# Performance work log

Hardware: AMD Instinct MI355X
Metric: run time of the kernel (lower is better)

Reference implementation:

```python
import jax, jax.numpy as jnp
import numpy as np

UNITS = 2048
BATCH = 4096
INPUT_DIM = 2048

def hard_sigmoid(x):
    # Keras hard_sigmoid: clip(0.2*x + 0.5, 0, 1)
    return jnp.clip(0.2 * x + 0.5, 0.0, 1.0)

def setup_inputs() -> dict:
    key = jax.random.key(0)
    ks = jax.random.split(key, 8)
    inputs = jax.random.normal(ks[0], (BATCH, INPUT_DIM), dtype=jnp.float32)
    h_tm1 = jax.random.normal(ks[1], (BATCH, UNITS), dtype=jnp.float32)
    c_tm1 = jax.random.normal(ks[2], (BATCH, UNITS), dtype=jnp.float32)
    z_tm1 = jax.random.normal(ks[3], (BATCH, UNITS), dtype=jnp.float32)
    scale = 1.0 / np.sqrt(INPUT_DIM)
    kernel = jax.random.normal(ks[4], (INPUT_DIM, 4 * UNITS), dtype=jnp.float32) * scale
    recurrent_kernel = jax.random.normal(ks[5], (UNITS, 4 * UNITS), dtype=jnp.float32) * scale
    recurrent_latent = jax.random.normal(ks[6], (UNITS, 4 * UNITS), dtype=jnp.float32) * scale
    # unit_forget_bias: bias = [zeros(units), ones(units), zeros(2*units)]
    bias = jnp.concatenate([
        jnp.zeros((UNITS,), jnp.float32),
        jnp.ones((UNITS,), jnp.float32),
        jnp.zeros((2 * UNITS,), jnp.float32),
    ])
    return {"inputs": inputs, "h_tm1": h_tm1, "c_tm1": c_tm1, "z_tm1": z_tm1,
            "kernel": kernel, "recurrent_kernel": recurrent_kernel,
            "recurrent_latent": recurrent_latent, "bias": bias}

def reference(inputs, h_tm1, c_tm1, z_tm1, kernel, recurrent_kernel, recurrent_latent, bias):
    # Fused path (implementation=2, no dropout): three matmuls + bias,
    # split into 4 gates, then gated state update.
    x = inputs @ kernel + h_tm1 @ recurrent_kernel + z_tm1 @ recurrent_latent + bias
    x_i, x_f, x_c, x_o = jnp.split(x, 4, axis=1)
    i = hard_sigmoid(x_i)
    f = hard_sigmoid(x_f)
    c = f * c_tm1 + i * jnp.tanh(x_c)
    o = hard_sigmoid(x_o)
    h = o * jnp.tanh(c)
    return h
```

## Files before the change

### kernel.cpp

```cpp
#include <hip/hip_runtime.h>
#include <hip/hip_bf16.h>

typedef float f32x4 __attribute__((ext_vector_type(4)));
typedef short short8 __attribute__((ext_vector_type(8)));
typedef short short4v __attribute__((ext_vector_type(4)));

__device__ __forceinline__ short f2b(float x) {
    union { __hip_bfloat16 b; short s; } u;
    u.b = __float2bfloat16(x);
    return u.s;
}

__device__ __forceinline__ void gload16(const void* g, void* l) {
    __builtin_amdgcn_global_load_lds(
        (const __attribute__((address_space(1))) unsigned int*)g,
        (__attribute__((address_space(3))) unsigned int*)l, 16, 0, 0);
}

__global__ __launch_bounds__(256)
void conv_a(const float* __restrict__ x0, const float* __restrict__ x1,
            const float* __restrict__ x2, unsigned short* __restrict__ Aws)
{
    const long i = (long)blockIdx.x * 256 + threadIdx.x;
    const long per_src = (long)4096 * 2048 / 8;
    const int  s = (int)(i / per_src);
    const long e0 = (i % per_src) * 8;
    const int  row = (int)(e0 >> 11), kl = (int)(e0 & 2047);
    const float* src = (s == 0) ? x0 : (s == 1) ? x1 : x2;
    const f32x4 v0 = *(const f32x4*)(src + e0);
    const f32x4 v1 = *(const f32x4*)(src + e0 + 4);
    short8 p;
    #pragma unroll
    for (int j = 0; j < 4; ++j) { p[j] = f2b(v0[j]); p[4 + j] = f2b(v1[j]); }
    *(short8*)&Aws[(long)row * 6144 + s * 2048 + kl] = p;
}

__global__ __launch_bounds__(256)
void conv_b(const float* __restrict__ Wk, const float* __restrict__ Wr,
            const float* __restrict__ Wl, unsigned short* __restrict__ Bws)
{
    __shared__ float lt[64][65];
    const int bid = (int)blockIdx.x;
    const int s   = bid >> 12;
    const int r   = bid & 4095;
    const int kbase = (r >> 7) * 64;
    const int ebase = (r & 127) * 64;
    const float* W = (s == 0) ? Wk : (s == 1) ? Wr : Wl;
    const int tr = threadIdx.x >> 4, tc = threadIdx.x & 15;

    #pragma unroll
    for (int p = 0; p < 4; ++p) {
        const int kr = p * 16 + tr;
        const f32x4 v = *(const f32x4*)&W[(long)(kbase + kr) * 8192 + ebase + tc * 4];
        #pragma unroll
        for (int j = 0; j < 4; ++j) lt[kr][tc * 4 + j] = v[j];
    }
    __syncthreads();
    #pragma unroll
    for (int p = 0; p < 4; ++p) {
        const int er = p * 16 + tr;
        const int k4 = tc * 4;
        short4v qv;
        #pragma unroll
        for (int j = 0; j < 4; ++j) qv[j] = f2b(lt[k4 + j][er]);
        *(short4v*)&Bws[(long)(ebase + er) * 6144 + (long)s * 2048 + kbase + k4] = qv;
    }
}

__global__ __launch_bounds__(512, 2)
void vlstm_gemm256(const unsigned short* __restrict__ Aws,
                   const unsigned short* __restrict__ Bws,
                   const float* __restrict__ c_tm1,
                   const float* __restrict__ bias,
                   float* __restrict__ out)
{
    __shared__ __align__(16) unsigned short As[2][256][64];
    __shared__ __align__(16) unsigned short Bs[3][256][64];

    const int tid  = threadIdx.x;
    const int w    = tid >> 6, lane = tid & 63;
    const int wm   = w >> 2,  wn   = w & 3;
    const int l15  = lane & 15, q = lane >> 4;
    const int lrow = lane >> 3;
    const int lsw  = (lane & 7) ^ lrow;
    const int oq   = q ^ (l15 & 7);

    const int bid = (int)blockIdx.x;
    const int swz = (bid & 7) * 64 + (bid >> 3);
    const int bm  = swz >> 5, bn = swz & 31;
    const int row0 = bm * 256, c0 = bn * 64;

    const long a_base = (long)(row0 + w * 16 + lrow) * 6144 + lsw * 8;

    f32x4 acc[8][4];
    #pragma unroll
    for (int mi = 0; mi < 8; ++mi)
        #pragma unroll
        for (int g = 0; g < 4; ++g)
            acc[mi][g] = (f32x4){0.f, 0.f, 0.f, 0.f};

    short8 afr[4][2];
    short8 bfr[4][2];

#define STAGE_A(buf_, t_, h_) do { _Pragma("unroll")                             \
    for (int j_ = 0; j_ < 2; ++j_)                                               \
        gload16(Aws + a_base + (long)((h_) * 128 + j_ * 8) * 6144                \
                    + (long)(t_) * 64,                                           \
                &As[buf_][(h_) * 128 + w * 16 + j_ * 8][0]); } while (0)

#define STAGE_B(buf_, t_, h_) do { _Pragma("unroll")                             \
    for (int j_ = 0; j_ < 2; ++j_) {                                             \
        const int e0_ = (h_) * 128 + w * 16 + j_ * 8;                            \
        const int grow_ = ((e0_ >> 4) & 3) * 2048 + c0 + (e0_ >> 6) * 16         \
                          + (e0_ & 8) + lrow;                                    \
        gload16(Bws + (long)grow_ * 6144 + lsw * 8 + (long)(t_) * 64,            \
                &Bs[buf_][e0_][0]); } } while (0)

#define LOAD_AFR(cur_, mh_) do { _Pragma("unroll")                               \
    for (int mi_ = 0; mi_ < 4; ++mi_) { _Pragma("unroll")                        \
        for (int kh_ = 0; kh_ < 2; ++kh_)                                        \
            afr[mi_][kh_] = *(const short8*)                                     \
                &As[cur_][wm * 128 + (mh_) * 64 + mi_ * 16 + l15]                \
                         [(oq ^ (kh_ << 2)) * 8]; } } while (0)

#define LOAD_BFR(cur_, nlo_) do { _Pragma("unroll")                              \
    for (int g_ = 0; g_ < 2; ++g_) { _Pragma("unroll")                           \
        for (int kh_ = 0; kh_ < 2; ++kh_)                                        \
            bfr[(nlo_) + g_][kh_] = *(const short8*)                             \
                &Bs[cur_][wn * 64 + ((nlo_) + g_) * 16 + l15]                    \
                         [(oq ^ (kh_ << 2)) * 8]; } } while (0)

#define MFMA_Q(mh_, nlo_) do {                                                   \
    __builtin_amdgcn_s_setprio(1);                                               \
    _Pragma("unroll")                                                            \
    for (int kh_ = 0; kh_ < 2; ++kh_) { _Pragma("unroll")                        \
        for (int mi_ = 0; mi_ < 4; ++mi_) { _Pragma("unroll")                    \
            for (int g_ = 0; g_ < 2; ++g_)                                       \
                acc[(mh_) * 4 + mi_][(nlo_) + g_] =                              \
                    __builtin_amdgcn_mfma_f32_16x16x32_bf16(                     \
                        afr[mi_][kh_], bfr[(nlo_) + g_][kh_],                    \
                        acc[(mh_) * 4 + mi_][(nlo_) + g_], 0, 0, 0); } }         \
    __builtin_amdgcn_s_setprio(0); } while (0)

#define BARRIER() do { __builtin_amdgcn_sched_barrier(0);                        \
    __builtin_amdgcn_s_barrier();                                                \
    __builtin_amdgcn_sched_barrier(0); } while (0)

    STAGE_A(0, 0, 0); STAGE_A(0, 0, 1);
    STAGE_B(0, 0, 0); STAGE_B(0, 0, 1);
    STAGE_B(1, 1, 0); STAGE_B(1, 1, 1);
    asm volatile("s_waitcnt vmcnt(4)" ::: "memory");
    BARRIER();

    int bB = 0;
    for (int t = 0; t < 96; ++t) {
        const int bA = t & 1, bAn = bA ^ 1;
        const int bBs = bB ? bB - 1 : 2;
        LOAD_AFR(bA, 0);
        LOAD_BFR(bB, 0);
        if (t + 1 < 96) STAGE_A(bAn, t + 1, 0);
        MFMA_Q(0, 0);
        LOAD_BFR(bB, 2);
        if (t + 1 < 96) STAGE_A(bAn, t + 1, 1);
        MFMA_Q(0, 2);
        LOAD_AFR(bA, 1);
        if (t + 2 < 96) STAGE_B(bBs, t + 2, 0);
        MFMA_Q(1, 0);
        if (t + 2 < 96) STAGE_B(bBs, t + 2, 1);
        MFMA_Q(1, 2);
        if (t < 94) asm volatile("s_waitcnt vmcnt(4)" ::: "memory");
        else        asm volatile("s_waitcnt vmcnt(0)" ::: "memory");
        BARRIER();
        bB = (bB == 2) ? 0 : bB + 1;
    }

#undef STAGE_A
#undef STAGE_B
#undef LOAD_AFR
#undef LOAD_BFR
#undef MFMA_Q
#undef BARRIER

    {
        const int col = c0 + wn * 16 + l15;
        const float bi  = bias[col];
        const float bf_ = bias[2048 + col];
        const float bc  = bias[4096 + col];
        const float bo  = bias[6144 + col];
        #pragma unroll
        for (int mi = 0; mi < 8; ++mi) {
            const int rbase = row0 + wm * 128 + mi * 16 + q * 4;
            #pragma unroll
            for (int rr = 0; rr < 4; ++rr) {
                const int row = rbase + rr;
                const float xi = acc[mi][0][rr] + bi;
                const float xf = acc[mi][1][rr] + bf_;
                const float xc = acc[mi][2][rr] + bc;
                const float xo = acc[mi][3][rr] + bo;
                const float ig = __builtin_amdgcn_fmed3f(0.2f * xi + 0.5f, 0.f, 1.f);
                const float fg = __builtin_amdgcn_fmed3f(0.2f * xf + 0.5f, 0.f, 1.f);
                const float og = __builtin_amdgcn_fmed3f(0.2f * xo + 0.5f, 0.f, 1.f);
                const float cp = c_tm1[(long)row * 2048 + col];
                const float cc = fg * cp + ig * tanhf(xc);
                out[(long)row * 2048 + col] = og * tanhf(cc);
            }
        }
    }
}

__global__ __launch_bounds__(256, 2)
void vlstm_fused_legacy(const float* __restrict__ xin, const float* __restrict__ h_tm1,
                        const float* __restrict__ c_tm1, const float* __restrict__ z_tm1,
                        const float* __restrict__ Wk, const float* __restrict__ Wr,
                        const float* __restrict__ Wl, const float* __restrict__ bias,
                        float* __restrict__ out)
{
    __shared__ __align__(16) unsigned short Alds[2][128][40];
    __shared__ __align__(16) unsigned short Blds[2][256][40];

    const int tid  = threadIdx.x;
    const int wave = tid >> 6, lane = tid & 63;
    const int wr = wave >> 1, wc = wave & 1;
    const int l15 = lane & 15, q = lane >> 4;

    const int bid = (int)blockIdx.x;
    const int swz = (bid & 7) * 128 + (bid >> 3);
    const int bm = swz >> 5, bn = swz & 31;
    const int row0 = bm * 128, col0 = bn * 64;

    const int arow = tid >> 1, kh = tid & 1;
    const long bg_off = (long)(tid >> 6) * 2048 + col0 + (tid & 63);

    f32x4 acc[4][4][2];
    #pragma unroll
    for (int g = 0; g < 4; ++g)
        #pragma unroll
        for (int mi = 0; mi < 4; ++mi)
            #pragma unroll
            for (int ni = 0; ni < 2; ++ni)
                acc[g][mi][ni] = (f32x4){0.f, 0.f, 0.f, 0.f};

    f32x4 sa[4];
    float sb[32];

#define DO_LOADS_L(kn_) do {                                                    \
    const int s_  = (kn_) >> 6;                                                 \
    const int kl_ = ((kn_) & 63) << 5;                                          \
    const float* Ap_ = (s_ == 0) ? xin : (s_ == 1) ? h_tm1 : z_tm1;             \
    const float* Bp_ = (s_ == 0) ? Wk  : (s_ == 1) ? Wr    : Wl;                \
    const float* ap_ = Ap_ + (long)(row0 + arow) * 2048 + kl_ + kh * 16;        \
    _Pragma("unroll")                                                           \
    for (int i_ = 0; i_ < 4; ++i_) sa[i_] = ((const f32x4*)ap_)[i_];            \
    const float* bp_ = Bp_ + (long)kl_ * 8192 + bg_off;                         \
    _Pragma("unroll")                                                           \
    for (int kk_ = 0; kk_ < 32; ++kk_) sb[kk_] = bp_[(long)kk_ * 8192];         \
} while (0)

#define DO_STORE_L(buf_) do {                                                   \
    short8 p0_, p1_;                                                            \
    _Pragma("unroll")                                                           \
    for (int j_ = 0; j_ < 4; ++j_) {                                            \
        p0_[j_] = f2b(sa[0][j_]); p0_[4 + j_] = f2b(sa[1][j_]);                 \
        p1_[j_] = f2b(sa[2][j_]); p1_[4 + j_] = f2b(sa[3][j_]);                 \
    }                                                                           \
    *(short8*)&Alds[buf_][arow][kh * 16]     = p0_;                             \
    *(short8*)&Alds[buf_][arow][kh * 16 + 8] = p1_;                             \
    _Pragma("unroll")                                                           \
    for (int ks_ = 0; ks_ < 4; ++ks_) {                                         \
        short8 pb_;                                                             \
        _Pragma("unroll")                                                       \
        for (int j_ = 0; j_ < 8; ++j_) pb_[j_] = f2b(sb[ks_ * 8 + j_]);         \
        *(short8*)&Blds[buf_][tid][ks_ * 8] = pb_;                              \
    }                                                                           \
} while (0)

    DO_LOADS_L(0);
    DO_STORE_L(0);
    __syncthreads();

    for (int kt = 0; kt < 192; ++kt) {
        const int cur = kt & 1;
        if (kt + 1 < 192) DO_LOADS_L(kt + 1);

        short8 afr[4];
        #pragma unroll
        for (int mi = 0; mi < 4; ++mi)
            afr[mi] = *(const short8*)&Alds[cur][wr * 64 + mi * 16 + l15][q * 8];

        short8 bfr[4][2];
        #pragma unroll
        for (int g = 0; g < 4; ++g)
            #pragma unroll
            for (int ni = 0; ni < 2; ++ni)
                bfr[g][ni] = *(const short8*)
                    &Blds[cur][g * 64 + wc * 32 + ni * 16 + l15][q * 8];

        #pragma unroll
        for (int g = 0; g < 4; ++g)
            #pragma unroll
            for (int ni = 0; ni < 2; ++ni)
                #pragma unroll
                for (int mi = 0; mi < 4; ++mi)
                    acc[g][mi][ni] = __builtin_amdgcn_mfma_f32_16x16x32_bf16(
                        afr[mi], bfr[g][ni], acc[g][mi][ni], 0, 0, 0);

        if (kt + 1 < 192) DO_STORE_L(cur ^ 1);
        __syncthreads();
    }

#undef DO_LOADS_L
#undef DO_STORE_L

    #pragma unroll
    for (int ni = 0; ni < 2; ++ni) {
        const int col = col0 + wc * 32 + ni * 16 + l15;
        const float bi  = bias[col];
        const float bf_ = bias[2048 + col];
        const float bc  = bias[4096 + col];
        const float bo  = bias[6144 + col];
        #pragma unroll
        for (int mi = 0; mi < 4; ++mi) {
            const int rbase = row0 + wr * 64 + mi * 16 + q * 4;
            #pragma unroll
            for (int rr = 0; rr < 4; ++rr) {
                const int row = rbase + rr;
                const float xi = acc[0][mi][ni][rr] + bi;
                const float xf = acc[1][mi][ni][rr] + bf_;
                const float xc = acc[2][mi][ni][rr] + bc;
                const float xo = acc[3][mi][ni][rr] + bo;
                const float ig = __builtin_amdgcn_fmed3f(0.2f * xi + 0.5f, 0.f, 1.f);
                const float fg = __builtin_amdgcn_fmed3f(0.2f * xf + 0.5f, 0.f, 1.f);
                const float og = __builtin_amdgcn_fmed3f(0.2f * xo + 0.5f, 0.f, 1.f);
                const float cp = c_tm1[(long)row * 2048 + col];
                const float cc = fg * cp + ig * tanhf(xc);
                out[(long)row * 2048 + col] = og * tanhf(cc);
            }
        }
    }
}

extern "C" void kernel_launch(void* const* d_in, const int* in_sizes, int n_in,
                              void* d_out, int out_size, void* d_ws, size_t ws_size,
                              hipStream_t stream) {
    const float* xin  = (const float*)d_in[0];
    const float* h1   = (const float*)d_in[1];
    const float* c1   = (const float*)d_in[2];
    const float* z1   = (const float*)d_in[3];
    const float* Wk   = (const float*)d_in[4];
    const float* Wr   = (const float*)d_in[5];
    const float* Wl   = (const float*)d_in[6];
    const float* bias = (const float*)d_in[7];
    float* out = (float*)d_out;
    (void)in_sizes; (void)n_in; (void)out_size;

    const size_t a_elems = (size_t)4096 * 6144;
    const size_t b_elems = (size_t)8192 * 6144;
    const size_t need = (a_elems + b_elems) * 2;

    if (ws_size >= need) {
        unsigned short* Aws = (unsigned short*)d_ws;
        unsigned short* Bws = Aws + a_elems;
        conv_a<<<dim3(12288), dim3(256), 0, stream>>>(xin, h1, z1, Aws);
        conv_b<<<dim3(12288), dim3(256), 0, stream>>>(Wk, Wr, Wl, Bws);
        vlstm_gemm256<<<dim3(512), dim3(512), 0, stream>>>(Aws, Bws, c1, bias, out);
    } else {
        vlstm_fused_legacy<<<dim3(1024), dim3(256), 0, stream>>>(
            xin, h1, c1, z1, Wk, Wr, Wl, bias, out);
    }
}
```

Baseline: 497.9 us.

## Load B fragments directly from global into registers, dropping B LDS staging

B tiles are no longer staged through shared memory. Each wave now loads its B MFMA fragments straight from global memory into a double-buffered register bank (b0/b1), prefetched one K-step ahead, and the loop is unrolled by two to alternate the banks. This removes the 96KB Bs LDS buffer and the LDS reads for B, which could improve occupancy and cut LDS traffic. The cost is that the four waves sharing the same wn now each fetch the same B data redundantly from global/L2, and register pressure rises.

```diff
diff --git a/kernel.cpp b/kernel.cpp
--- a/kernel.cpp
+++ b/kernel.cpp
@@ -68,14 +68,13 @@
 }
 
 __global__ __launch_bounds__(512, 2)
-void vlstm_gemm256(const unsigned short* __restrict__ Aws,
+void vlstm_gemm_bd(const unsigned short* __restrict__ Aws,
                    const unsigned short* __restrict__ Bws,
                    const float* __restrict__ c_tm1,
                    const float* __restrict__ bias,
                    float* __restrict__ out)
 {
     __shared__ __align__(16) unsigned short As[2][256][64];
-    __shared__ __align__(16) unsigned short Bs[3][256][64];
 
     const int tid  = threadIdx.x;
     const int w    = tid >> 6, lane = tid & 63;
@@ -92,6 +91,14 @@
 
     const long a_base = (long)(row0 + w * 16 + lrow) * 6144 + lsw * 8;
 
+    const unsigned short* bpg[4];
+    {
+        const unsigned short* bp0 =
+            Bws + ((long)(c0 + wn * 16 + l15) * 6144 + q * 8);
+        #pragma unroll
+        for (int g = 0; g < 4; ++g) bpg[g] = bp0 + (long)g * (2048 * 6144);
+    }
+
     f32x4 acc[8][4];
     #pragma unroll
     for (int mi = 0; mi < 8; ++mi)
@@ -100,7 +107,7 @@
             acc[mi][g] = (f32x4){0.f, 0.f, 0.f, 0.f};
 
     short8 afr[4][2];
-    short8 bfr[4][2];
+    short8 b0[4][2], b1[4][2];
 
 #define STAGE_A(buf_, t_, h_) do { _Pragma("unroll")                             \
     for (int j_ = 0; j_ < 2; ++j_)                                               \
@@ -108,13 +115,11 @@
                     + (long)(t_) * 64,                                           \
                 &As[buf_][(h_) * 128 + w * 16 + j_ * 8][0]); } while (0)
 
-#define STAGE_B(buf_, t_, h_) do { _Pragma("unroll")                             \
-    for (int j_ = 0; j_ < 2; ++j_) {                                             \
-        const int e0_ = (h_) * 128 + w * 16 + j_ * 8;                            \
-        const int grow_ = ((e0_ >> 4) & 3) * 2048 + c0 + (e0_ >> 6) * 16         \
-                          + (e0_ & 8) + lrow;                                    \
-        gload16(Bws + (long)grow_ * 6144 + lsw * 8 + (long)(t_) * 64,            \
-                &Bs[buf_][e0_][0]); } } while (0)
+#define BLOADS(bank_, t_) do { _Pragma("unroll")                                 \
+    for (int g_ = 0; g_ < 4; ++g_) {                                             \
+        bank_[g_][0] = *(const short8*)(bpg[g_] + (long)(t_) * 64);              \
+        bank_[g_][1] = *(const short8*)(bpg[g_] + (long)(t_) * 64 + 32);         \
+    } } while (0)
 
 #define LOAD_AFR(cur_, mh_) do { _Pragma("unroll")                               \
     for (int mi_ = 0; mi_ < 4; ++mi_) { _Pragma("unroll")                        \
@@ -123,14 +128,7 @@
                 &As[cur_][wm * 128 + (mh_) * 64 + mi_ * 16 + l15]                \
                          [(oq ^ (kh_ << 2)) * 8]; } } while (0)
 
-#define LOAD_BFR(cur_, nlo_) do { _Pragma("unroll")                              \
-    for (int g_ = 0; g_ < 2; ++g_) { _Pragma("unroll")                           \
-        for (int kh_ = 0; kh_ < 2; ++kh_)                                        \
-            bfr[(nlo_) + g_][kh_] = *(const short8*)                             \
-                &Bs[cur_][wn * 64 + ((nlo_) + g_) * 16 + l15]                    \
-                         [(oq ^ (kh_ << 2)) * 8]; } } while (0)
-
-#define MFMA_Q(mh_, nlo_) do {                                                   \
+#define MFMA_Q(bank_, mh_, nlo_) do {                                            \
     __builtin_amdgcn_s_setprio(1);                                               \
     _Pragma("unroll")                                                            \
     for (int kh_ = 0; kh_ < 2; ++kh_) { _Pragma("unroll")                        \
@@ -138,7 +136,7 @@
             for (int g_ = 0; g_ < 2; ++g_)                                       \
                 acc[(mh_) * 4 + mi_][(nlo_) + g_] =                              \
                     __builtin_amdgcn_mfma_f32_16x16x32_bf16(                     \
-                        afr[mi_][kh_], bfr[(nlo_) + g_][kh_],                    \
+                        afr[mi_][kh_], bank_[(nlo_) + g_][kh_],                  \
                         acc[(mh_) * 4 + mi_][(nlo_) + g_], 0, 0, 0); } }         \
     __builtin_amdgcn_s_setprio(0); } while (0)
 
@@ -146,40 +144,40 @@
     __builtin_amdgcn_s_barrier();                                                \
     __builtin_amdgcn_sched_barrier(0); } while (0)
 
-    STAGE_A(0, 0, 0); STAGE_A(0, 0, 1);
-    STAGE_B(0, 0, 0); STAGE_B(0, 0, 1);
-    STAGE_B(1, 1, 0); STAGE_B(1, 1, 1);
-    asm volatile("s_waitcnt vmcnt(4)" ::: "memory");
+#define TILE_BODY(cur_, nxt_, t_) do {                                           \
+    const int bufA_ = (t_) & 1;                                                  \
+    LOAD_AFR(bufA_, 0);                                                          \
+    if ((t_) + 1 < 96) {                                                         \
+        STAGE_A(bufA_ ^ 1, (t_) + 1, 0);                                         \
+        STAGE_A(bufA_ ^ 1, (t_) + 1, 1);                                         \
+        BLOADS(nxt_, (t_) + 1);                                                  \
+    }                                                                            \
+    MFMA_Q(cur_, 0, 0);                                                          \
+    MFMA_Q(cur_, 0, 2);                                                          \
+    LOAD_AFR(bufA_, 1);                                                          \
+    MFMA_Q(cur_, 1, 0);                                                          \
+    MFMA_Q(cur_, 1, 2);                                                          \
+    if ((t_) < 94) asm volatile("s_waitcnt vmcnt(8)" ::: "memory");              \
+    else           asm volatile("s_waitcnt vmcnt(0)" ::: "memory");              \
+    BARRIER(); } while (0)
+
+    STAGE_A(0, 0, 0);
+    STAGE_A(0, 0, 1);
+    BLOADS(b0, 0);
+    asm volatile("s_waitcnt vmcnt(0)" ::: "memory");
     BARRIER();
 
-    int bB = 0;
-    for (int t = 0; t < 96; ++t) {
-        const int bA = t & 1, bAn = bA ^ 1;
-        const int bBs = bB ? bB - 1 : 2;
-        LOAD_AFR(bA, 0);
-        LOAD_BFR(bB, 0);
-        if (t + 1 < 96) STAGE_A(bAn, t + 1, 0);
-        MFMA_Q(0, 0);
-        LOAD_BFR(bB, 2);
-        if (t + 1 < 96) STAGE_A(bAn, t + 1, 1);
-        MFMA_Q(0, 2);
-        LOAD_AFR(bA, 1);
-        if (t + 2 < 96) STAGE_B(bBs, t + 2, 0);
-        MFMA_Q(1, 0);
-        if (t + 2 < 96) STAGE_B(bBs, t + 2, 1);
-        MFMA_Q(1, 2);
-        if (t < 94) asm volatile("s_waitcnt vmcnt(4)" ::: "memory");
-        else        asm volatile("s_waitcnt vmcnt(0)" ::: "memory");
-        BARRIER();
-        bB = (bB == 2) ? 0 : bB + 1;
+    for (int t2 = 0; t2 < 96; t2 += 2) {
+        TILE_BODY(b0, b1, t2);
+        TILE_BODY(b1, b0, t2 + 1);
     }
 
 #undef STAGE_A
-#undef STAGE_B
+#undef BLOADS
 #undef LOAD_AFR
-#undef LOAD_BFR
 #undef MFMA_Q
 #undef BARRIER
+#undef TILE_BODY
 
     {
         const int col = c0 + wn * 16 + l15;
@@ -362,7 +360,7 @@
         unsigned short* Bws = Aws + a_elems;
         conv_a<<<dim3(12288), dim3(256), 0, stream>>>(xin, h1, z1, Aws);
         conv_b<<<dim3(12288), dim3(256), 0, stream>>>(Wk, Wr, Wl, Bws);
-        vlstm_gemm256<<<dim3(512), dim3(512), 0, stream>>>(Aws, Bws, c1, bias, out);
+        vlstm_gemm_bd<<<dim3(512), dim3(512), 0, stream>>>(Aws, Bws, c1, bias, out);
     } else {
         vlstm_fused_legacy<<<dim3(1024), dim3(256), 0, stream>>>(
             xin, h1, c1, z1, Wk, Wr, Wl, bias, out);
```

Result: slower. 647.8 us (+30.1%).
